# Kernel optimization log

Measured on AMD Instinct MI355X. Metric: run time of the kernel, lower is better.

The kernel has to match this reference:

```python
import jax, jax.numpy as jnp
import numpy as np

B, C, H, W = 32, 512, 32, 32


def setup_inputs() -> dict:
    key = jax.random.key(0)
    ks = jax.random.split(key, 7)
    c2 = C // 2
    s_in = (1.0 / C) ** 0.5   # torch Conv2d default init scale (kernel 1x1)
    s_c2 = (1.0 / c2) ** 0.5
    return {
        "x": jax.random.normal(ks[0], (B, C, H, W), jnp.float32),
        "Wk": jax.random.normal(ks[1], (c2, C), jnp.float32) * s_in,
        "bk": jax.random.normal(ks[2], (c2,), jnp.float32) * s_in,
        "Wv": jax.random.normal(ks[3], (c2, C), jnp.float32) * s_in,
        "bv": jax.random.normal(ks[4], (c2,), jnp.float32) * s_in,
        "Wo": jax.random.normal(ks[5], (C, c2), jnp.float32) * s_c2,
        "bo": jax.random.normal(ks[6], (C,), jnp.float32) * s_c2,
    }


def reference(x, Wk, bk, Wv, bv, Wo, bo):
    Bn, Cn, Hn, Wn = x.shape
    c2 = Cn // 2
    M = Hn * Wn
    # 1x1 convs as channel contractions
    k = jnp.einsum('oc,bchw->bohw', Wk, x) + bk[None, :, None, None]   # [B,c2,H,W]
    v = jnp.einsum('oc,bchw->bohw', Wv, x) + bv[None, :, None, None]   # [B,c2,H,W]
    # torch .reshape(B, M, c2) reinterprets memory (NOT a transpose) -> same in jnp
    v = v.reshape(Bn, M, c2)                                           # [B,M,c2]
    kf = k.reshape(Bn, c2, M)                                          # [B,c2,M]
    # cov_feature: k^T I_hat k with I_hat = (1/M)I - (1/M^2)11^T
    #            = (1/M) k^T k - (1/M^2) s s^T,  s = sum over channels
    gram = jnp.einsum('bcm,bcn->bmn', kf, kf) / M                      # [B,M,M]
    s = kf.sum(axis=1)                                                 # [B,M]
    cov = gram - (s[:, :, None] * s[:, None, :]) / (M * M)
    attn = jax.nn.softmax(cov * (c2 ** -0.5), axis=-1)                 # [B,M,M]
    out = jnp.einsum('bmn,bnc->bmc', attn, v)                          # [B,M,c2]
    # torch .view(B, c2, H, W) is also a raw memory reinterpretation
    out = out.reshape(Bn, c2, Hn, Wn)
    out = jnp.einsum('oc,bchw->bohw', Wo, out) + bo[None, :, None, None]
    return out + x
```

## Files before the change

### kernel.cpp

```cpp
#include <hip/hip_runtime.h>


typedef short bf8 __attribute__((ext_vector_type(8)));
typedef float f32x4 __attribute__((ext_vector_type(4)));

#define MFMA16(a, b, c) __builtin_amdgcn_mfma_f32_16x16x32_bf16((a), (b), (c), 0, 0, 0)

__device__ __forceinline__ short f2bf(float x) {
  unsigned u = __float_as_uint(x);
  u += 0x7fffu + ((u >> 16) & 1u);
  return (short)(u >> 16);
}

__device__ __forceinline__ void gll16(const short* g, void* l) {
  __builtin_amdgcn_global_load_lds(
      (const __attribute__((address_space(1))) unsigned int*)g,
      (__attribute__((address_space(3))) unsigned int*)l, 16, 0, 0);
}

__device__ __forceinline__ void gemm_core(const short* __restrict__ A,
                                          const short* __restrict__ B,
                                          int ldA, int ldB, int ksteps,
                                          char* smem, f32x4 acc[4][4]) {
  const int tid = threadIdx.x;
  const int w = tid >> 6, l = tid & 63;
  const int q = l >> 4, i = l & 15;
  const int wm = w & 1, wn = w >> 1;
  const int srow = l >> 3;
  const int gcol = ((l & 7) ^ srow) * 8;
  f32x4 zz = {0.f, 0.f, 0.f, 0.f};
  #pragma unroll
  for (int mt = 0; mt < 4; ++mt)
    #pragma unroll
    for (int nt = 0; nt < 4; ++nt) acc[mt][nt] = zz;

  for (int ks = 0; ks < ksteps; ++ks) {
    __syncthreads();
    const short* Ak = A + ks * 64 + gcol;
    const short* Bk = B + ks * 64 + gcol;
    #pragma unroll
    for (int j = 0; j < 4; ++j) {
      int s = w * 4 + j;
      size_t row = (size_t)(s * 8 + srow);
      gll16(Ak + row * ldA, smem + s * 1024);
      gll16(Bk + row * ldB, smem + 16384 + s * 1024);
    }
    __syncthreads();
    #pragma unroll
    for (int kq = 0; kq < 2; ++kq) {
      int sw = ((kq * 4 + q) ^ (i & 7)) * 16;
      bf8 af[4], bq[4];
      #pragma unroll
      for (int mt = 0; mt < 4; ++mt)
        af[mt] = *(const bf8*)(smem + (wm * 64 + mt * 16 + i) * 128 + sw);
      #pragma unroll
      for (int nt = 0; nt < 4; ++nt)
        bq[nt] = *(const bf8*)(smem + 16384 + (wn * 64 + nt * 16 + i) * 128 + sw);
      #pragma unroll
      for (int mt = 0; mt < 4; ++mt)
        #pragma unroll
        for (int nt = 0; nt < 4; ++nt)
          acc[mt][nt] = MFMA16(af[mt], bq[nt], acc[mt][nt]);
    }
  }
}

__global__ __launch_bounds__(256) void p0_xpose(const float* __restrict__ x,
                                                short* __restrict__ xT) {
  __shared__ float lds[64][65];
  int cb = blockIdx.x, sb = blockIdx.y, b = blockIdx.z;
  int t = threadIdx.x;
  int c0 = cb * 64, sp0 = sb * 64;
  const float4* x4 = reinterpret_cast<const float4*>(x);
  #pragma unroll
  for (int j = 0; j < 4; ++j) {
    int lin = t + 256 * j;
    int cl = lin >> 4, s4 = lin & 15;
    float4 v = x4[(((size_t)b * 512 + c0 + cl) * 1024 + sp0 + s4 * 4) >> 2];
    lds[cl][s4 * 4 + 0] = v.x; lds[cl][s4 * 4 + 1] = v.y;
    lds[cl][s4 * 4 + 2] = v.z; lds[cl][s4 * 4 + 3] = v.w;
  }
  __syncthreads();
  int spl = t >> 2, cs = (t & 3) * 16;
  bf8 o0, o1;
  #pragma unroll
  for (int j = 0; j < 8; ++j) o0[j] = f2bf(lds[cs + j][spl]);
  #pragma unroll
  for (int j = 0; j < 8; ++j) o1[j] = f2bf(lds[cs + 8 + j][spl]);
  size_t base = ((size_t)b * 1024 + sp0 + spl) * 512 + c0 + cs;
  *reinterpret_cast<bf8*>(xT + base) = o0;
  *reinterpret_cast<bf8*>(xT + base + 8) = o1;
}

__global__ __launch_bounds__(256) void w0_weights(const float* __restrict__ Wk,
                                                  const float* __restrict__ Wv,
                                                  const float* __restrict__ Wo,
                                                  short* __restrict__ Wkv_bf,
                                                  short* __restrict__ Wo_bf) {
  int g = blockIdx.x * 256 + threadIdx.x;
  if (g < 262144) {
    int o = g >> 9, c = g & 511;
    float v = (o < 256) ? Wk[o * 512 + c] : Wv[(o - 256) * 512 + c];
    Wkv_bf[g] = f2bf(v);
  } else {
    int i2 = g - 262144;
    Wo_bf[i2] = f2bf(Wo[i2]);
  }
}

__global__ __launch_bounds__(256, 2) void k1_kv(const short* __restrict__ xT,
                                                const short* __restrict__ Wkv,
                                                const float* __restrict__ bk,
                                                const float* __restrict__ bv,
                                                short* __restrict__ kT,
                                                short* __restrict__ vT,
                                                float* __restrict__ s_part) {
  __shared__ __attribute__((aligned(16))) char smem[32768];
  f32x4 acc[4][4];
  int bm = blockIdx.x, bn = blockIdx.y;
  gemm_core(xT + (size_t)bm * 128 * 512, Wkv + (size_t)bn * 128 * 512,
            512, 512, 8, smem, acc);
  int tid = threadIdx.x;
  int w = tid >> 6, l = tid & 63, q = l >> 4, i = l & 15;
  int wm = w & 1, wn = w >> 1;
  int mbase = bm * 128 + wm * 64;
  int nbase = bn * 128 + wn * 64;
  if (bn < 2) {
    float rp[4][4];
    #pragma unroll
    for (int mt = 0; mt < 4; ++mt)
      #pragma unroll
      for (int r = 0; r < 4; ++r) rp[mt][r] = 0.f;
    #pragma unroll
    for (int mt = 0; mt < 4; ++mt)
      #pragma unroll
      for (int nt = 0; nt < 4; ++nt) {
        float bias = bk[nbase + nt * 16 + i];
        #pragma unroll
        for (int r = 0; r < 4; ++r) {
          float val = acc[mt][nt][r] + bias;
          int mg = mbase + mt * 16 + q * 4 + r;
          kT[(size_t)mg * 256 + nbase + nt * 16 + i] = f2bf(val);
          rp[mt][r] += val;
        }
      }
    #pragma unroll
    for (int mask = 1; mask <= 8; mask <<= 1)
      #pragma unroll
      for (int mt = 0; mt < 4; ++mt)
        #pragma unroll
        for (int r = 0; r < 4; ++r) rp[mt][r] += __shfl_xor(rp[mt][r], mask, 64);
    if (i == 0) {
      int pg = bn * 2 + wn;
      #pragma unroll
      for (int mt = 0; mt < 4; ++mt)
        #pragma unroll
        for (int r = 0; r < 4; ++r)
          s_part[pg * 32768 + mbase + mt * 16 + q * 4 + r] = rp[mt][r];
    }
  } else {
    #pragma unroll
    for (int mt = 0; mt < 4; ++mt)
      #pragma unroll
      for (int nt = 0; nt < 4; ++nt) {
        int o2 = nbase + nt * 16 + i - 256;
        float bias = bv[o2];
        #pragma unroll
        for (int r = 0; r < 4; ++r) {
          float val = acc[mt][nt][r] + bias;
          int mg = mbase + mt * 16 + q * 4 + r;
          int b = mg >> 10, sp = mg & 1023;
          vT[((size_t)b * 256 + (sp & 255)) * 1024 + 4 * o2 + (sp >> 8)] = f2bf(val);
        }
      }
  }
}

__global__ __launch_bounds__(256) void k1b_sum(const float* __restrict__ s_part,
                                               float* __restrict__ s_buf) {
  int t = blockIdx.x * 256 + threadIdx.x;
  s_buf[t] = s_part[t] + s_part[32768 + t] + s_part[65536 + t] + s_part[98304 + t];
}

__global__ __launch_bounds__(256, 2) void k2_fused(const short* __restrict__ kT,
                                                   const short* __restrict__ vT,
                                                   const float* __restrict__ s_buf,
                                                   short* __restrict__ OB) {
  __shared__ __attribute__((aligned(16))) char smem[81920];
  char* Apan = smem;
  char* Ppan = smem + 32768;
  char* Bst  = smem + 49152;

  const int bm = blockIdx.x, b = blockIdx.y;
  const int tid = threadIdx.x;
  const int w = tid >> 6, l = tid & 63;
  const int q = l >> 4, i = l & 15;
  const int srow = l >> 3;
  const int gcol = ((l & 7) ^ srow) * 8;

  const short* kTb = kT + (size_t)b * 1024 * 256;
  const short* vTb = vT + (size_t)b * 256 * 1024;
  const float* sB = s_buf + b * 1024;

  {
    const short* Am = kTb + (size_t)bm * 64 * 256;
    #pragma unroll
    for (int ks = 0; ks < 4; ++ks)
      #pragma unroll
      for (int j2 = 0; j2 < 2; ++j2) {
        int s2 = w * 2 + j2;
        gll16(Am + (size_t)(s2 * 8 + srow) * 256 + ks * 64 + gcol,
              Apan + ks * 8192 + s2 * 1024);
      }
  }

  float sm[4][4];
  #pragma unroll
  for (int mt = 0; mt < 4; ++mt)
    #pragma unroll
    for (int r = 0; r < 4; ++r) sm[mt][r] = sB[bm * 64 + mt * 16 + q * 4 + r];

  f32x4 zz = {0.f, 0.f, 0.f, 0.f};
  f32x4 acc_o[4][4];
  #pragma unroll
  for (int mt = 0; mt < 4; ++mt)
    #pragma unroll
    for (int ct = 0; ct < 4; ++ct) acc_o[mt][ct] = zz;
  float rowsum[4][4];
  #pragma unroll
  for (int mt = 0; mt < 4; ++mt)
    #pragma unroll
    for (int r = 0; r < 4; ++r) rowsum[mt][r] = 0.f;

  const float sc1 = 1.0f / 16384.0f;
  const float sc2 = 1.0f / 16777216.0f;

  for (int n0 = 0; n0 < 1024; n0 += 128) {
    f32x4 acc_s[4][2];
    #pragma unroll
    for (int mt = 0; mt < 4; ++mt)
      #pragma unroll
      for (int nt = 0; nt < 2; ++nt) acc_s[mt][nt] = zz;
    const short* Bn = kTb + (size_t)n0 * 256;
    for (int ks = 0; ks < 4; ++ks) {
      __syncthreads();
      #pragma unroll
      for (int j = 0; j < 4; ++j) {
        int s = w * 4 + j;
        gll16(Bn + (size_t)(s * 8 + srow) * 256 + ks * 64 + gcol, Bst + s * 1024);
      }
      __syncthreads();
      #pragma unroll
      for (int kq = 0; kq < 2; ++kq) {
        int sw = ((kq * 4 + q) ^ (i & 7)) * 16;
        bf8 af[4], bq2[2];
        #pragma unroll
        for (int mt = 0; mt < 4; ++mt)
          af[mt] = *(const bf8*)(Apan + ks * 8192 + (mt * 16 + i) * 128 + sw);
        #pragma unroll
        for (int nt = 0; nt < 2; ++nt)
          bq2[nt] = *(const bf8*)(Bst + (w * 32 + nt * 16 + i) * 128 + sw);
        #pragma unroll
        for (int mt = 0; mt < 4; ++mt)
          #pragma unroll
          for (int nt = 0; nt < 2; ++nt)
            acc_s[mt][nt] = MFMA16(af[mt], bq2[nt], acc_s[mt][nt]);
      }
    }
    float sn0 = sB[n0 + w * 32 + i];
    float sn1 = sB[n0 + w * 32 + 16 + i];
    #pragma unroll
    for (int nt = 0; nt < 2; ++nt) {
      float sn = nt ? sn1 : sn0;
      int nl = w * 32 + nt * 16 + i;
      char* pbase = Ppan + (nl >> 6) * 8192 + (nl & 7) * 2;
      int gchunk = (nl >> 3) & 7;
      #pragma unroll
      for (int mt = 0; mt < 4; ++mt)
        #pragma unroll
        for (int r = 0; r < 4; ++r) {
          int ml = mt * 16 + q * 4 + r;
          float p = __expf(acc_s[mt][nt][r] * sc1 - sm[mt][r] * sn * sc2);
          rowsum[mt][r] += p;
          *(short*)(pbase + ml * 128 + ((gchunk ^ (ml & 7)) * 16)) = f2bf(p);
        }
    }
    for (int ks2 = 0; ks2 < 2; ++ks2) {
      __syncthreads();
      #pragma unroll
      for (int j = 0; j < 8; ++j) {
        int s = w * 8 + j;
        gll16(vTb + (size_t)(s * 8 + srow) * 1024 + n0 + ks2 * 64 + gcol,
              Bst + s * 1024);
      }
      __syncthreads();
      #pragma unroll
      for (int kq = 0; kq < 2; ++kq) {
        int sw = ((kq * 4 + q) ^ (i & 7)) * 16;
        bf8 ap[4], bv4[4];
        #pragma unroll
        for (int mt = 0; mt < 4; ++mt)
          ap[mt] = *(const bf8*)(Ppan + ks2 * 8192 + (mt * 16 + i) * 128 + sw);
        #pragma unroll
        for (int ct = 0; ct < 4; ++ct)
          bv4[ct] = *(const bf8*)(Bst + (w * 64 + ct * 16 + i) * 128 + sw);
        #pragma unroll
        for (int mt = 0; mt < 4; ++mt)
          #pragma unroll
          for (int ct = 0; ct < 4; ++ct)
            acc_o[mt][ct] = MFMA16(ap[mt], bv4[ct], acc_o[mt][ct]);
      }
    }
  }
  #pragma unroll
  for (int mask = 1; mask <= 8; mask <<= 1)
    #pragma unroll
    for (int mt = 0; mt < 4; ++mt)
      #pragma unroll
      for (int r = 0; r < 4; ++r) rowsum[mt][r] += __shfl_xor(rowsum[mt][r], mask, 64);
  __syncthreads();
  float* rs = (float*)Ppan;
  if (i == 0) {
    #pragma unroll
    for (int mt = 0; mt < 4; ++mt)
      #pragma unroll
      for (int r = 0; r < 4; ++r)
        rs[w * 64 + mt * 16 + q * 4 + r] = rowsum[mt][r];
  }
  __syncthreads();
  float rinv[4][4];
  #pragma unroll
  for (int mt = 0; mt < 4; ++mt)
    #pragma unroll
    for (int r = 0; r < 4; ++r) {
      int m = mt * 16 + q * 4 + r;
      rinv[mt][r] = 1.0f / (rs[m] + rs[64 + m] + rs[128 + m] + rs[192 + m]);
    }
  short* ob = (short*)(Bst + w * 8192);
  #pragma unroll
  for (int mt = 0; mt < 4; ++mt)
    #pragma unroll
    for (int ct = 0; ct < 4; ++ct)
      #pragma unroll
      for (int r = 0; r < 4; ++r)
        ob[(r * 64 + ct * 16 + i) * 16 + mt * 4 + q] =
            f2bf(acc_o[mt][ct][r] * rinv[mt][r]);
  short* obg = OB + (size_t)b * 1024 * 256;
  #pragma unroll
  for (int jj = 0; jj < 8; ++jj) {
    int lr = jj * 32 + (l >> 1), ch = l & 1;
    bf8 vv = *(const bf8*)(ob + lr * 16 + ch * 8);
    int rr = lr >> 6, cc = lr & 63;
    *(bf8*)(obg + ((size_t)(rr * 256 + w * 64 + cc)) * 256 + bm * 16 + ch * 8) = vv;
  }
}

__global__ __launch_bounds__(256, 2) void k3_out(const short* __restrict__ Wo_bf,
                                                 const short* __restrict__ OB,
                                                 const float* __restrict__ bo,
                                                 const float* __restrict__ x,
                                                 float* __restrict__ out) {
  __shared__ __attribute__((aligned(16))) char smem[32768];
  f32x4 acc[4][4];
  int bm = blockIdx.x, bn = blockIdx.y, b = blockIdx.z;
  gemm_core(Wo_bf + (size_t)bm * 128 * 256,
            OB + ((size_t)b * 1024 + bn * 128) * 256, 256, 256, 4, smem, acc);
  int tid = threadIdx.x;
  int w = tid >> 6, l = tid & 63, q = l >> 4, i = l & 15;
  int wm = w & 1, wn = w >> 1;
  int oloc = bm * 128 + wm * 64, sploc = bn * 128 + wn * 64;
  #pragma unroll
  for (int mt = 0; mt < 4; ++mt)
    #pragma unroll
    for (int r = 0; r < 4; ++r) {
      int o = oloc + mt * 16 + q * 4 + r;
      float bias = bo[o];
      #pragma unroll
      for (int nt = 0; nt < 4; ++nt) {
        int sp = sploc + nt * 16 + i;
        size_t idx = ((size_t)b * 512 + o) * 1024 + sp;
        out[idx] = acc[mt][nt][r] + bias + x[idx];
      }
    }
}

extern "C" void kernel_launch(void* const* d_in, const int* in_sizes, int n_in,
                              void* d_out, int out_size, void* d_ws, size_t ws_size,
                              hipStream_t stream) {
  (void)in_sizes; (void)n_in; (void)out_size; (void)ws_size;
  const float* x  = (const float*)d_in[0];
  const float* Wk = (const float*)d_in[1];
  const float* bk = (const float*)d_in[2];
  const float* Wv = (const float*)d_in[3];
  const float* bv = (const float*)d_in[4];
  const float* Wo = (const float*)d_in[5];
  const float* bo = (const float*)d_in[6];
  float* out = (float*)d_out;
  char* ws = (char*)d_ws;

  short* xT     = (short*)(ws);
  short* OB     = (short*)(ws);
  short* kTb    = (short*)(ws + 33554432);
  short* vTb    = (short*)(ws + 50331648);
  short* Wkv_bf = (short*)(ws + 67108864);
  short* Wo_bf  = (short*)(ws + 67633152);
  float* s_part = (float*)(ws + 67895296);
  float* s_buf  = (float*)(ws + 68419584);

  p0_xpose<<<dim3(8, 16, 32), 256, 0, stream>>>(x, xT);
  w0_weights<<<1536, 256, 0, stream>>>(Wk, Wv, Wo, Wkv_bf, Wo_bf);
  k1_kv<<<dim3(256, 4), 256, 0, stream>>>(xT, Wkv_bf, bk, bv, kTb, vTb, s_part);
  k1b_sum<<<128, 256, 0, stream>>>(s_part, s_buf);
  k2_fused<<<dim3(16, 32), 256, 0, stream>>>(kTb, vTb, s_buf, OB);
  k3_out<<<dim3(4, 8, 32), 256, 0, stream>>>(Wo_bf, OB, bo, x, out);
}
```

Measured before the change: 252.2 us.

## Double-buffer K and V tiles in attention loop with unified prefetch schedule

Flattens the per-n0 K-gram and PV stages into one 64-step loop. Each step prefetches the next 16KB K or V slice into an alternate LDS buffer while the current slice is consumed, so one barrier per step replaces two. The V tile is now split into two channel halves per step, and the output staging is rewritten to use the whole shared buffer. The cost is more LDS for buffering and extra control flow inside the loop.

New measurement: 415.8 us. 64.9% more time.

```diff
diff --git a/kernel.cpp b/kernel.cpp
--- a/kernel.cpp
+++ b/kernel.cpp
@@ -213,6 +213,11 @@
               Apan + ks * 8192 + s2 * 1024);
       }
   }
+  #pragma unroll
+  for (int j = 0; j < 4; ++j) {
+    int s = w * 4 + j;
+    gll16(kTb + (size_t)(s * 8 + srow) * 256 + gcol, Bst + s * 1024);
+  }
 
   float sm[4][4];
   #pragma unroll
@@ -226,6 +231,7 @@
   for (int mt = 0; mt < 4; ++mt)
     #pragma unroll
     for (int ct = 0; ct < 4; ++ct) acc_o[mt][ct] = zz;
+  f32x4 acc_s[4][2];
   float rowsum[4][4];
   #pragma unroll
   for (int mt = 0; mt < 4; ++mt)
@@ -235,80 +241,91 @@
   const float sc1 = 1.0f / 16384.0f;
   const float sc2 = 1.0f / 16777216.0f;
 
-  for (int n0 = 0; n0 < 1024; n0 += 128) {
-    f32x4 acc_s[4][2];
-    #pragma unroll
-    for (int mt = 0; mt < 4; ++mt)
-      #pragma unroll
-      for (int nt = 0; nt < 2; ++nt) acc_s[mt][nt] = zz;
-    const short* Bn = kTb + (size_t)n0 * 256;
-    for (int ks = 0; ks < 4; ++ks) {
-      __syncthreads();
-      #pragma unroll
-      for (int j = 0; j < 4; ++j) {
-        int s = w * 4 + j;
-        gll16(Bn + (size_t)(s * 8 + srow) * 256 + ks * 64 + gcol, Bst + s * 1024);
-      }
-      __syncthreads();
+  for (int g = 0; g < 64; ++g) {
+    const int gs = g & 7;
+    const int n0 = (g >> 3) * 128;
+    __syncthreads();
+    if (g < 63) {
+      const int g1 = g + 1, gs1 = g1 & 7, n1 = (g1 >> 3) * 128;
+      char* nb = Bst + (g1 & 1) * 16384;
+      if (gs1 < 4) {
+        #pragma unroll
+        for (int j = 0; j < 4; ++j) {
+          int s = w * 4 + j;
+          gll16(kTb + (size_t)(n1 + s * 8 + srow) * 256 + gs1 * 64 + gcol,
+                nb + s * 1024);
+        }
+      } else {
+        int kh = (gs1 - 4) >> 1, ch = (gs1 - 4) & 1;
+        #pragma unroll
+        for (int j = 0; j < 4; ++j) {
+          int s = w * 4 + j;
+          gll16(vTb + (size_t)(ch * 128 + s * 8 + srow) * 1024 + n1 + kh * 64 + gcol,
+                nb + s * 1024);
+        }
+      }
+    }
+    char* cb = Bst + (g & 1) * 16384;
+    if (gs < 4) {
+      if (gs == 0) {
+        #pragma unroll
+        for (int mt = 0; mt < 4; ++mt)
+          #pragma unroll
+          for (int nt = 0; nt < 2; ++nt) acc_s[mt][nt] = zz;
+      }
       #pragma unroll
       for (int kq = 0; kq < 2; ++kq) {
         int sw = ((kq * 4 + q) ^ (i & 7)) * 16;
         bf8 af[4], bq2[2];
         #pragma unroll
         for (int mt = 0; mt < 4; ++mt)
-          af[mt] = *(const bf8*)(Apan + ks * 8192 + (mt * 16 + i) * 128 + sw);
+          af[mt] = *(const bf8*)(Apan + gs * 8192 + (mt * 16 + i) * 128 + sw);
         #pragma unroll
         for (int nt = 0; nt < 2; ++nt)
-          bq2[nt] = *(const bf8*)(Bst + (w * 32 + nt * 16 + i) * 128 + sw);
+          bq2[nt] = *(const bf8*)(cb + (w * 32 + nt * 16 + i) * 128 + sw);
         #pragma unroll
         for (int mt = 0; mt < 4; ++mt)
           #pragma unroll
           for (int nt = 0; nt < 2; ++nt)
             acc_s[mt][nt] = MFMA16(af[mt], bq2[nt], acc_s[mt][nt]);
       }
-    }
-    float sn0 = sB[n0 + w * 32 + i];
-    float sn1 = sB[n0 + w * 32 + 16 + i];
-    #pragma unroll
-    for (int nt = 0; nt < 2; ++nt) {
-      float sn = nt ? sn1 : sn0;
-      int nl = w * 32 + nt * 16 + i;
-      char* pbase = Ppan + (nl >> 6) * 8192 + (nl & 7) * 2;
-      int gchunk = (nl >> 3) & 7;
-      #pragma unroll
-      for (int mt = 0; mt < 4; ++mt)
-        #pragma unroll
-        for (int r = 0; r < 4; ++r) {
-          int ml = mt * 16 + q * 4 + r;
-          float p = __expf(acc_s[mt][nt][r] * sc1 - sm[mt][r] * sn * sc2);
-          rowsum[mt][r] += p;
-          *(short*)(pbase + ml * 128 + ((gchunk ^ (ml & 7)) * 16)) = f2bf(p);
+      if (gs == 3) {
+        float sn0 = sB[n0 + w * 32 + i];
+        float sn1 = sB[n0 + w * 32 + 16 + i];
+        #pragma unroll
+        for (int nt = 0; nt < 2; ++nt) {
+          float sn = nt ? sn1 : sn0;
+          int nl = w * 32 + nt * 16 + i;
+          char* pbase = Ppan + (nl >> 6) * 8192 + (nl & 7) * 2;
+          int gchunk = (nl >> 3) & 7;
+          #pragma unroll
+          for (int mt = 0; mt < 4; ++mt)
+            #pragma unroll
+            for (int r = 0; r < 4; ++r) {
+              int ml = mt * 16 + q * 4 + r;
+              float p = __expf(acc_s[mt][nt][r] * sc1 - sm[mt][r] * sn * sc2);
+              rowsum[mt][r] += p;
+              *(short*)(pbase + ml * 128 + ((gchunk ^ (ml & 7)) * 16)) = f2bf(p);
+            }
         }
-    }
-    for (int ks2 = 0; ks2 < 2; ++ks2) {
-      __syncthreads();
-      #pragma unroll
-      for (int j = 0; j < 8; ++j) {
-        int s = w * 8 + j;
-        gll16(vTb + (size_t)(s * 8 + srow) * 1024 + n0 + ks2 * 64 + gcol,
-              Bst + s * 1024);
-      }
-      __syncthreads();
+      }
+    } else {
+      const int kh = (gs - 4) >> 1, ch = (gs - 4) & 1;
       #pragma unroll
       for (int kq = 0; kq < 2; ++kq) {
         int sw = ((kq * 4 + q) ^ (i & 7)) * 16;
-        bf8 ap[4], bv4[4];
+        bf8 ap[4], bv2[2];
         #pragma unroll
         for (int mt = 0; mt < 4; ++mt)
-          ap[mt] = *(const bf8*)(Ppan + ks2 * 8192 + (mt * 16 + i) * 128 + sw);
-        #pragma unroll
-        for (int ct = 0; ct < 4; ++ct)
-          bv4[ct] = *(const bf8*)(Bst + (w * 64 + ct * 16 + i) * 128 + sw);
+          ap[mt] = *(const bf8*)(Ppan + kh * 8192 + (mt * 16 + i) * 128 + sw);
+        #pragma unroll
+        for (int ct = 0; ct < 2; ++ct)
+          bv2[ct] = *(const bf8*)(cb + (w * 32 + ct * 16 + i) * 128 + sw);
         #pragma unroll
         for (int mt = 0; mt < 4; ++mt)
           #pragma unroll
-          for (int ct = 0; ct < 4; ++ct)
-            acc_o[mt][ct] = MFMA16(ap[mt], bv4[ct], acc_o[mt][ct]);
+          for (int ct = 0; ct < 2; ++ct)
+            acc_o[mt][ch * 2 + ct] = MFMA16(ap[mt], bv2[ct], acc_o[mt][ch * 2 + ct]);
       }
     }
   }
@@ -336,22 +353,24 @@
       int m = mt * 16 + q * 4 + r;
       rinv[mt][r] = 1.0f / (rs[m] + rs[64 + m] + rs[128 + m] + rs[192 + m]);
     }
-  short* ob = (short*)(Bst + w * 8192);
-  #pragma unroll
-  for (int mt = 0; mt < 4; ++mt)
-    #pragma unroll
-    for (int ct = 0; ct < 4; ++ct)
+  short* ob = (short*)Bst;
+  #pragma unroll
+  for (int mt = 0; mt < 4; ++mt)
+    #pragma unroll
+    for (int ctg = 0; ctg < 4; ++ctg) {
+      int cg = (ctg >> 1) * 128 + w * 32 + (ctg & 1) * 16 + i;
       #pragma unroll
       for (int r = 0; r < 4; ++r)
-        ob[(r * 64 + ct * 16 + i) * 16 + mt * 4 + q] =
-            f2bf(acc_o[mt][ct][r] * rinv[mt][r]);
+        ob[(r * 256 + cg) * 16 + mt * 4 + q] = f2bf(acc_o[mt][ctg][r] * rinv[mt][r]);
+    }
+  __syncthreads();
   short* obg = OB + (size_t)b * 1024 * 256;
   #pragma unroll
   for (int jj = 0; jj < 8; ++jj) {
-    int lr = jj * 32 + (l >> 1), ch = l & 1;
-    bf8 vv = *(const bf8*)(ob + lr * 16 + ch * 8);
-    int rr = lr >> 6, cc = lr & 63;
-    *(bf8*)(obg + ((size_t)(rr * 256 + w * 64 + cc)) * 256 + bm * 16 + ch * 8) = vv;
+    int lin = jj * 256 + tid;
+    int row = lin >> 1, chh = lin & 1;
+    *(bf8*)(obg + (size_t)row * 256 + bm * 16 + chh * 8) =
+        *(const bf8*)(ob + row * 16 + chh * 8);
   }
 }
 
```
